# Kernel tuning notes

Hardware: AMD Instinct MI355X
Metric: run time of the kernel (lower is better)

Reference implementation:

```python
import jax, jax.numpy as jnp
import numpy as np

B, L, CIN = 32768, 35, 21
N_FLANK, C_FLANK, PEP_MAX = 10, 10, 15
F, K, H = 128, 9, 64


def setup_inputs() -> dict:
    key = jax.random.key(0)
    ks = jax.random.split(key, 16)
    s = lambda k, shape, scale=0.05: jax.random.normal(k, shape, dtype=jnp.float32) * scale
    return {
        "sequence": jax.random.normal(ks[0], (B, L, CIN), dtype=jnp.float32),
        "peptide_length": jax.random.randint(ks[1], (B,), 5, PEP_MAX + 1, dtype=jnp.int32),
        # main conv, weight in WIO layout (k, in, out)
        "conv_w": s(ks[2], (K, CIN, F)),
        "conv_b": jnp.zeros((F,), jnp.float32),
        # n-flank post 1x1 convs (as matmuls)
        "n_w1": s(ks[3], (F, H)), "n_b1": jnp.zeros((H,), jnp.float32),
        "n_w2": s(ks[4], (H, 1)), "n_b2": jnp.zeros((1,), jnp.float32),
        # c-flank post 1x1 convs
        "c_w1": s(ks[5], (F, H)), "c_b1": jnp.zeros((H,), jnp.float32),
        "c_w2": s(ks[6], (H, 1)), "c_b2": jnp.zeros((1,), jnp.float32),
        # flank-average dense layers
        "navg_w": s(ks[7], (F, 1)), "navg_b": jnp.zeros((1,), jnp.float32),
        "cavg_w": s(ks[8], (F, 1)), "cavg_b": jnp.zeros((1,), jnp.float32),
        # output layer: init ones / zeros as in the torch module
        "out_w": jnp.ones((6, 1), jnp.float32),
        "out_b": jnp.zeros((1,), jnp.float32),
    }


def _post(x, w1, b1, w2, b2):
    # stack of 1x1 convs: relu on hidden, tanh on final single-output layer
    h = jax.nn.relu(jnp.einsum("blf,fh->blh", x, w1) + b1)
    return jnp.tanh(jnp.einsum("blh,ho->blo", h, w2) + b2)  # [B, L, 1]


def _masked_neg_max(y, mask):
    # torch: max over dim1 of (y+1)*mask, minus 1, negated
    m = mask[..., None].astype(y.dtype)
    return -(jnp.max((y + 1.0) * m, axis=1) - 1.0)  # [B, 1]


def reference(sequence, peptide_length, conv_w, conv_b, n_w1, n_b1, n_w2, n_b2,
              c_w1, c_b1, c_w2, c_b2, navg_w, navg_b, cavg_w, cavg_b, out_w, out_b):
    # main conv, padding='same', relu activation (dropout rate 0 -> no-op)
    x = jax.lax.conv_general_dilated(
        sequence, conv_w, window_strides=(1,), padding="SAME",
        dimension_numbers=("NWC", "WIO", "NWC"))
    conv_result = jax.nn.relu(x + conv_b)  # [B, L, F]

    plen = peptide_length.reshape(-1)
    pos = jnp.arange(L)[None, :]  # [1, L]

    # --- n-flank branch ---
    yn = _post(conv_result, n_w1, n_b1, n_w2, n_b2)  # [B, L, 1]
    cleaved_n = yn[:, N_FLANK, :]  # [B, 1]
    mask_n = (pos >= N_FLANK + 1) & (pos < (N_FLANK + plen)[:, None])
    maxpool_n = _masked_neg_max(yn, mask_n)
    avg_n = jnp.tanh(jnp.mean(conv_result[:, :N_FLANK], axis=1) @ navg_w + navg_b)

    # --- c-flank branch ---
    yc = _post(conv_result, c_w1, c_b1, c_w2, c_b2)  # [B, L, 1]
    c_idx = (N_FLANK + plen - 1).astype(jnp.int32)
    cleaved_c = jnp.take_along_axis(yc, c_idx[:, None, None], axis=1)[:, 0, :]  # [B, 1]
    mask_c = (pos >= N_FLANK) & (pos < (N_FLANK + plen - 1)[:, None])
    maxpool_c = _masked_neg_max(yc, mask_c)
    starts = (N_FLANK + plen)[:, None]
    mask_cf = ((pos >= starts) & (pos < starts + C_FLANK))[..., None].astype(conv_result.dtype)
    s = jnp.sum((conv_result + 1.0) * mask_cf, axis=1)  # [B, F]
    cnt = jnp.clip(jnp.sum(mask_cf, axis=1), 1.0, None)
    avg_c = jnp.tanh((s / cnt - 1.0) @ cavg_w + cavg_b)

    combined = jnp.concatenate(
        [cleaved_n, maxpool_n, avg_n, cleaved_c, maxpool_c, avg_c], axis=-1)  # [B, 6]
    out = jax.nn.sigmoid(combined @ out_w + out_b)
    return out[:, 0]  # [B]
```

## Files before the change

### kernel.cpp

```cpp
#include <hip/hip_runtime.h>
#include <hip/hip_bf16.h>
#include <math.h>

#define Ln     35
#define CINn   21
#define CINP   24
#define Fn     128
#define Kn     9
#define Hn     64
#define GB     16
#define SEQ_STRIDE 1064
#define TILE_STRIDE 136
#define YP_STRIDE 136
#define NYL    16

typedef __attribute__((ext_vector_type(8))) short short8;
typedef __attribute__((ext_vector_type(4))) float f32x4;

static __device__ __forceinline__ unsigned short bf16bits(float f) {
    __hip_bfloat16 h = __float2bfloat16(f);
    return *(unsigned short*)&h;
}

template <int CTRL>
static __device__ __forceinline__ float dpp_add(float v) {
    int r = __builtin_amdgcn_update_dpp(0, __builtin_bit_cast(int, v),
                                        CTRL, 0xF, 0xF, true);
    return v + __builtin_bit_cast(float, r);
}
static __device__ __forceinline__ float row_sum16(float v) {
    v = dpp_add<0x128>(v);
    v = dpp_add<0x124>(v);
    v = dpp_add<0x122>(v);
    v = dpp_add<0x121>(v);
    return v;
}

__global__ __launch_bounds__(512, 4) void fused_kernel(
    const float* __restrict__ seq,    const int*   __restrict__ plen_arr,
    const float* __restrict__ conv_w, const float* __restrict__ conv_b,
    const float* __restrict__ n_w1,   const float* __restrict__ n_b1,
    const float* __restrict__ n_w2,   const float* __restrict__ n_b2,
    const float* __restrict__ c_w1,   const float* __restrict__ c_b1,
    const float* __restrict__ c_w2,   const float* __restrict__ c_b2,
    const float* __restrict__ navg_w, const float* __restrict__ navg_b,
    const float* __restrict__ cavg_w, const float* __restrict__ cavg_b,
    const float* __restrict__ out_w,  const float* __restrict__ out_b,
    float* __restrict__ out)
{
    __shared__ __align__(16) unsigned short s_seq[GB * SEQ_STRIDE];
    __shared__ __align__(16) unsigned short s_tile[4][GB * TILE_STRIDE];
    __shared__ __align__(16) float s_yp[NYL * YP_STRIDE];
    float* s_y   = (float*)s_seq;
    float* s_avg = (float*)s_seq + 1152;

    const int t    = threadIdx.x;
    const int wave = t >> 6;
    const int lane = t & 63;
    const int quad = lane >> 4;
    const int col  = lane & 15;
    const int b0   = blockIdx.x * GB;

    {
        uint4* p = (uint4*)s_seq;
        for (int i = t; i < (GB * SEQ_STRIDE) / 8; i += 512)
            p[i] = make_uint4(0u, 0u, 0u, 0u);
    }

    short8 wb[7];
    short8 w1b[4];
    float  cbias[4], b1v, w2v;
    const int head = wave >> 2;
    {
        const int ng = wave * 16 + col;
        #pragma unroll
        for (int s = 0; s < 7; s++) {
            short8 v;
            #pragma unroll
            for (int j = 0; j < 8; j++) {
                int kk = 32 * s + quad * 8 + j;
                int k = kk / CINP, c = kk % CINP;
                float f = (k < Kn && c < CINn) ? conv_w[(k * CINn + c) * Fn + ng] : 0.0f;
                v[j] = (short)bf16bits(f);
            }
            wb[s] = v;
        }
        const int nl = ng & 63;
        #pragma unroll
        for (int s = 0; s < 4; s++) {
            short8 v;
            #pragma unroll
            for (int j = 0; j < 8; j++) {
                int k = 32 * s + quad * 8 + j;
                float f = head ? c_w1[k * Hn + nl] : n_w1[k * Hn + nl];
                v[j] = (short)bf16bits(f);
            }
            w1b[s] = v;
        }
        #pragma unroll
        for (int r = 0; r < 4; r++)
            cbias[r] = conv_b[wave * 16 + 4 * quad + r];
        b1v = head ? c_b1[nl] : n_b1[nl];
        w2v = head ? c_w2[nl] : n_w2[nl];
    }
    const int plen_lane = plen_arr[b0 + col];

    __syncthreads();

    {
        const float4* gsrc = (const float4*)(seq + (size_t)b0 * (Ln * CINn));
        for (int i = t; i < (GB * Ln * CINn) / 4; i += 512) {
            int i4 = i * 4;
            int bi = i4 / (Ln * CINn), r = i4 - bi * (Ln * CINn);
            int l = r / CINn, c = r - l * CINn;
            float4 v = gsrc[i];
            int base = bi * SEQ_STRIDE + (4 + l) * CINP + c;
            #pragma unroll
            for (int j = 0; j < 4; j++) {
                float fj = (j == 0) ? v.x : (j == 1) ? v.y : (j == 2) ? v.z : v.w;
                int adj = ((c + j >= CINn) ? 3 : 0) + ((r + j >= Ln * CINn) ? 224 : 0);
                s_seq[base + j + adj] = bf16bits(fj);
            }
        }
    }
    __syncthreads();

    float sum_n[4] = {0.f,0.f,0.f,0.f};
    float sum_c[4] = {0.f,0.f,0.f,0.f};

    for (int l0 = 0; l0 < 36; l0 += 2) {
        const int l1 = l0 + 1;
        short8 af0[7], af1[7];
        #pragma unroll
        for (int s = 0; s < 7; s++) {
            af0[s] = *(const short8*)&s_seq[col * SEQ_STRIDE + l0 * CINP + 32 * s + quad * 8];
            af1[s] = *(const short8*)&s_seq[col * SEQ_STRIDE + l1 * CINP + 32 * s + quad * 8];
        }
        f32x4 cacc0 = {0.f,0.f,0.f,0.f};
        f32x4 cacc1 = {0.f,0.f,0.f,0.f};
        #pragma unroll
        for (int s = 0; s < 7; s++) {
            cacc0 = __builtin_amdgcn_mfma_f32_16x16x32_bf16(wb[s], af0[s], cacc0, 0, 0, 0);
            cacc1 = __builtin_amdgcn_mfma_f32_16x16x32_bf16(wb[s], af1[s], cacc1, 0, 0, 0);
        }
        float a0 = fmaxf(cacc0[0] + cbias[0], 0.0f);
        float a1 = fmaxf(cacc0[1] + cbias[1], 0.0f);
        float a2 = fmaxf(cacc0[2] + cbias[2], 0.0f);
        float a3 = fmaxf(cacc0[3] + cbias[3], 0.0f);
        float e0 = fmaxf(cacc1[0] + cbias[0], 0.0f);
        float e1 = fmaxf(cacc1[1] + cbias[1], 0.0f);
        float e2 = fmaxf(cacc1[2] + cbias[2], 0.0f);
        float e3 = fmaxf(cacc1[3] + cbias[3], 0.0f);
        {
            float cm0 = (l0 >= 10 + plen_lane && l0 < 20 + plen_lane) ? 1.0f : 0.0f;
            float cm1 = (l1 >= 10 + plen_lane && l1 < 20 + plen_lane) ? 1.0f : 0.0f;
            if (l0 < 10) {
                sum_n[0] += a0; sum_n[1] += a1; sum_n[2] += a2; sum_n[3] += a3;
            }
            if (l1 < 10) {
                sum_n[0] += e0; sum_n[1] += e1; sum_n[2] += e2; sum_n[3] += e3;
            }
            sum_c[0] += cm0 * a0 + cm1 * e0;
            sum_c[1] += cm0 * a1 + cm1 * e1;
            sum_c[2] += cm0 * a2 + cm1 * e2;
            sum_c[3] += cm0 * a3 + cm1 * e3;
        }

        if (l0 >= 10 && l0 < 26) {
            ushort4 pk0 = { bf16bits(a0), bf16bits(a1), bf16bits(a2), bf16bits(a3) };
            ushort4 pk1 = { bf16bits(e0), bf16bits(e1), bf16bits(e2), bf16bits(e3) };
            *(ushort4*)&s_tile[l0 & 3][col * TILE_STRIDE + wave * 16 + 4 * quad] = pk0;
            *(ushort4*)&s_tile[l1 & 3][col * TILE_STRIDE + wave * 16 + 4 * quad] = pk1;
            __syncthreads();

            short8 am0[4], am1[4];
            #pragma unroll
            for (int s = 0; s < 4; s++) {
                am0[s] = *(const short8*)&s_tile[l0 & 3][col * TILE_STRIDE + 32 * s + quad * 8];
                am1[s] = *(const short8*)&s_tile[l1 & 3][col * TILE_STRIDE + 32 * s + quad * 8];
            }
            f32x4 hacc0 = {0.f,0.f,0.f,0.f};
            f32x4 hacc1 = {0.f,0.f,0.f,0.f};
            #pragma unroll
            for (int s = 0; s < 4; s++) {
                hacc0 = __builtin_amdgcn_mfma_f32_16x16x32_bf16(am0[s], w1b[s], hacc0, 0, 0, 0);
                hacc1 = __builtin_amdgcn_mfma_f32_16x16x32_bf16(am1[s], w1b[s], hacc1, 0, 0, 0);
            }
            float p0[4], p1[4];
            #pragma unroll
            for (int r = 0; r < 4; r++) {
                p0[r] = row_sum16(fmaxf(hacc0[r] + b1v, 0.f) * w2v);
                p1[r] = row_sum16(fmaxf(hacc1[r] + b1v, 0.f) * w2v);
            }
            if (col == 0) {
                *(f32x4*)&s_yp[(l0 - 10) * YP_STRIDE + wave * 16 + quad * 4] =
                    (f32x4){p0[0], p0[1], p0[2], p0[3]};
                *(f32x4*)&s_yp[(l1 - 10) * YP_STRIDE + wave * 16 + quad * 4] =
                    (f32x4){p1[0], p1[1], p1[2], p1[3]};
            }
        }
    }
    __syncthreads();

    {
        float an = 0.f, ac = 0.f;
        #pragma unroll
        for (int r = 0; r < 4; r++) {
            int fidx = wave * 16 + 4 * quad + r;
            an += sum_n[r] * navg_w[fidx];
            ac += sum_c[r] * cavg_w[fidx];
        }
        an += __shfl_xor(an, 16); an += __shfl_xor(an, 32);
        ac += __shfl_xor(ac, 16); ac += __shfl_xor(ac, 32);
        if (quad == 0) {
            s_avg[wave * 2 * GB + 0 * GB + col] = an;
            s_avg[wave * 2 * GB + 1 * GB + col] = ac;
        }
    }
    __syncthreads();

    {
        const float bn = n_b2[0], bc = c_b2[0];
        for (int i = t; i < 2 * GB * NYL; i += 512) {
            int m = i & 15, rem = i >> 4;
            int li = rem & 15, hd = rem >> 4;
            float v = (hd ? bc : bn);
            #pragma unroll
            for (int w = 0; w < 4; w++)
                v += s_yp[li * YP_STRIDE + (hd * 4 + w) * 16 + m];
            s_y[hd * GB * 36 + m * 36 + (10 + li)] = tanhf(v);
        }
    }
    __syncthreads();

    if (t < GB) {
        const int m = t;
        const int plen = plen_arr[b0 + m];
        const float* ym = s_y + m * 36;
        const float* yc = s_y + GB * 36 + m * 36;
        float cleaved_n = ym[10];
        float mn = 0.f;
        for (int l = 11; l < 10 + plen; l++) mn = fmaxf(mn, ym[l] + 1.f);
        float maxpool_n = -(mn - 1.f);
        float cleaved_c = yc[10 + plen - 1];
        float mc = 0.f;
        for (int l = 10; l < 10 + plen - 1; l++) mc = fmaxf(mc, yc[l] + 1.f);
        float maxpool_c = -(mc - 1.f);
        float sn = 0.f, sc = 0.f;
        #pragma unroll
        for (int w = 0; w < 8; w++) {
            sn += s_avg[w * 2 * GB + 0 * GB + m];
            sc += s_avg[w * 2 * GB + 1 * GB + m];
        }
        float avg_n = tanhf(sn * 0.1f + navg_b[0]);
        float avg_c = tanhf(sc * 0.1f + cavg_b[0]);
        float comb = cleaved_n * out_w[0] + maxpool_n * out_w[1] + avg_n * out_w[2]
                   + cleaved_c * out_w[3] + maxpool_c * out_w[4] + avg_c * out_w[5]
                   + out_b[0];
        out[b0 + m] = 1.f / (1.f + expf(-comb));
    }
}

extern "C" void kernel_launch(void* const* d_in, const int* in_sizes, int n_in,
                              void* d_out, int out_size, void* d_ws, size_t ws_size,
                              hipStream_t stream) {
    const int B = in_sizes[1];
    fused_kernel<<<B / GB, 512, 0, stream>>>(
        (const float*)d_in[0],  (const int*)d_in[1],
        (const float*)d_in[2],  (const float*)d_in[3],
        (const float*)d_in[4],  (const float*)d_in[5],
        (const float*)d_in[6],  (const float*)d_in[7],
        (const float*)d_in[8],  (const float*)d_in[9],
        (const float*)d_in[10], (const float*)d_in[11],
        (const float*)d_in[12], (const float*)d_in[13],
        (const float*)d_in[14], (const float*)d_in[15],
        (const float*)d_in[16], (const float*)d_in[17],
        (float*)d_out);
}
```

Before: 304.9 us.

## Software-pipeline hidden-layer MFMA behind conv with 8-slot tile ring

Grows the shared-memory activation ring from 4 to 8 slots and delays the hidden-layer MFMA consumer by two iterations, so a barrier is needed only every other iteration instead of every iteration in the window. The conv and hidden MFMA bias adds are folded into the accumulator initial values, and the c-flank mask test becomes a single unsigned compare. This trades extra LDS (which may reduce occupancy) and a more complex schedule for fewer block-wide syncs.

```diff
diff --git a/kernel.cpp b/kernel.cpp
--- a/kernel.cpp
+++ b/kernel.cpp
@@ -49,7 +49,7 @@
     float* __restrict__ out)
 {
     __shared__ __align__(16) unsigned short s_seq[GB * SEQ_STRIDE];
-    __shared__ __align__(16) unsigned short s_tile[4][GB * TILE_STRIDE];
+    __shared__ __align__(16) unsigned short s_tile[8][GB * TILE_STRIDE];
     __shared__ __align__(16) float s_yp[NYL * YP_STRIDE];
     float* s_y   = (float*)s_seq;
     float* s_avg = (float*)s_seq + 1152;
@@ -136,30 +136,28 @@
             af0[s] = *(const short8*)&s_seq[col * SEQ_STRIDE + l0 * CINP + 32 * s + quad * 8];
             af1[s] = *(const short8*)&s_seq[col * SEQ_STRIDE + l1 * CINP + 32 * s + quad * 8];
         }
-        f32x4 cacc0 = {0.f,0.f,0.f,0.f};
-        f32x4 cacc1 = {0.f,0.f,0.f,0.f};
+        f32x4 cacc0 = {cbias[0], cbias[1], cbias[2], cbias[3]};
+        f32x4 cacc1 = {cbias[0], cbias[1], cbias[2], cbias[3]};
         #pragma unroll
         for (int s = 0; s < 7; s++) {
             cacc0 = __builtin_amdgcn_mfma_f32_16x16x32_bf16(wb[s], af0[s], cacc0, 0, 0, 0);
             cacc1 = __builtin_amdgcn_mfma_f32_16x16x32_bf16(wb[s], af1[s], cacc1, 0, 0, 0);
         }
-        float a0 = fmaxf(cacc0[0] + cbias[0], 0.0f);
-        float a1 = fmaxf(cacc0[1] + cbias[1], 0.0f);
-        float a2 = fmaxf(cacc0[2] + cbias[2], 0.0f);
-        float a3 = fmaxf(cacc0[3] + cbias[3], 0.0f);
-        float e0 = fmaxf(cacc1[0] + cbias[0], 0.0f);
-        float e1 = fmaxf(cacc1[1] + cbias[1], 0.0f);
-        float e2 = fmaxf(cacc1[2] + cbias[2], 0.0f);
-        float e3 = fmaxf(cacc1[3] + cbias[3], 0.0f);
+        float a0 = fmaxf(cacc0[0], 0.0f);
+        float a1 = fmaxf(cacc0[1], 0.0f);
+        float a2 = fmaxf(cacc0[2], 0.0f);
+        float a3 = fmaxf(cacc0[3], 0.0f);
+        float e0 = fmaxf(cacc1[0], 0.0f);
+        float e1 = fmaxf(cacc1[1], 0.0f);
+        float e2 = fmaxf(cacc1[2], 0.0f);
+        float e3 = fmaxf(cacc1[3], 0.0f);
+        if (l0 < 10) {
+            sum_n[0] += a0 + e0; sum_n[1] += a1 + e1;
+            sum_n[2] += a2 + e2; sum_n[3] += a3 + e3;
+        }
         {
-            float cm0 = (l0 >= 10 + plen_lane && l0 < 20 + plen_lane) ? 1.0f : 0.0f;
-            float cm1 = (l1 >= 10 + plen_lane && l1 < 20 + plen_lane) ? 1.0f : 0.0f;
-            if (l0 < 10) {
-                sum_n[0] += a0; sum_n[1] += a1; sum_n[2] += a2; sum_n[3] += a3;
-            }
-            if (l1 < 10) {
-                sum_n[0] += e0; sum_n[1] += e1; sum_n[2] += e2; sum_n[3] += e3;
-            }
+            float cm0 = ((unsigned)(l0 - 10 - plen_lane) < 10u) ? 1.0f : 0.0f;
+            float cm1 = ((unsigned)(l1 - 10 - plen_lane) < 10u) ? 1.0f : 0.0f;
             sum_c[0] += cm0 * a0 + cm1 * e0;
             sum_c[1] += cm0 * a1 + cm1 * e1;
             sum_c[2] += cm0 * a2 + cm1 * e2;
@@ -169,18 +167,20 @@
         if (l0 >= 10 && l0 < 26) {
             ushort4 pk0 = { bf16bits(a0), bf16bits(a1), bf16bits(a2), bf16bits(a3) };
             ushort4 pk1 = { bf16bits(e0), bf16bits(e1), bf16bits(e2), bf16bits(e3) };
-            *(ushort4*)&s_tile[l0 & 3][col * TILE_STRIDE + wave * 16 + 4 * quad] = pk0;
-            *(ushort4*)&s_tile[l1 & 3][col * TILE_STRIDE + wave * 16 + 4 * quad] = pk1;
-            __syncthreads();
-
+            *(ushort4*)&s_tile[l0 & 7][col * TILE_STRIDE + wave * 16 + 4 * quad] = pk0;
+            *(ushort4*)&s_tile[l1 & 7][col * TILE_STRIDE + wave * 16 + 4 * quad] = pk1;
+        }
+
+        if (l0 >= 14 && l0 < 30) {
+            const int lp0 = l0 - 4, lp1 = l0 - 3;
             short8 am0[4], am1[4];
             #pragma unroll
             for (int s = 0; s < 4; s++) {
-                am0[s] = *(const short8*)&s_tile[l0 & 3][col * TILE_STRIDE + 32 * s + quad * 8];
-                am1[s] = *(const short8*)&s_tile[l1 & 3][col * TILE_STRIDE + 32 * s + quad * 8];
-            }
-            f32x4 hacc0 = {0.f,0.f,0.f,0.f};
-            f32x4 hacc1 = {0.f,0.f,0.f,0.f};
+                am0[s] = *(const short8*)&s_tile[lp0 & 7][col * TILE_STRIDE + 32 * s + quad * 8];
+                am1[s] = *(const short8*)&s_tile[lp1 & 7][col * TILE_STRIDE + 32 * s + quad * 8];
+            }
+            f32x4 hacc0 = {b1v, b1v, b1v, b1v};
+            f32x4 hacc1 = {b1v, b1v, b1v, b1v};
             #pragma unroll
             for (int s = 0; s < 4; s++) {
                 hacc0 = __builtin_amdgcn_mfma_f32_16x16x32_bf16(am0[s], w1b[s], hacc0, 0, 0, 0);
@@ -189,16 +189,19 @@
             float p0[4], p1[4];
             #pragma unroll
             for (int r = 0; r < 4; r++) {
-                p0[r] = row_sum16(fmaxf(hacc0[r] + b1v, 0.f) * w2v);
-                p1[r] = row_sum16(fmaxf(hacc1[r] + b1v, 0.f) * w2v);
+                p0[r] = row_sum16(fmaxf(hacc0[r], 0.f) * w2v);
+                p1[r] = row_sum16(fmaxf(hacc1[r], 0.f) * w2v);
             }
             if (col == 0) {
-                *(f32x4*)&s_yp[(l0 - 10) * YP_STRIDE + wave * 16 + quad * 4] =
+                *(f32x4*)&s_yp[(lp0 - 10) * YP_STRIDE + wave * 16 + quad * 4] =
                     (f32x4){p0[0], p0[1], p0[2], p0[3]};
-                *(f32x4*)&s_yp[(l1 - 10) * YP_STRIDE + wave * 16 + quad * 4] =
+                *(f32x4*)&s_yp[(lp1 - 10) * YP_STRIDE + wave * 16 + quad * 4] =
                     (f32x4){p1[0], p1[1], p1[2], p1[3]};
             }
         }
+
+        if (l0 >= 12 && l0 <= 24 && (l0 & 3) == 0)
+            __syncthreads();
     }
     __syncthreads();
 
```

Result: slower. 370.1 us (+21.4%).
